# Kernel optimization log

Measured on AMD Instinct MI355X. Metric: run time of the kernel, lower is better.

Reference implementation:

```python
import jax, jax.numpy as jnp
import numpy as np

B, N, D, NH, MAXLEN = 2, 2048, 1024, 16, 2048
HD = D // NH

def srel_skew(x):
    # x: [B, H, n, n] -> music-transformer skew
    b, h, n, _ = x.shape
    v = jnp.pad(x, ((0, 0), (0, 0), (0, 0), (1, 0)))  # pad last dim left
    return v.reshape(b, h, n + 1, n)[:, :, :n, :]

def split_head(x):
    # [B, n, D] -> [B, H, n, HD]
    b, n, _ = x.shape
    return x.reshape(b, n, NH, HD).transpose(0, 2, 1, 3)

def setup_inputs() -> dict:
    key = jax.random.key(0)
    ks = jax.random.split(key, 7)
    scale = 0.02
    return {
        "x": jax.random.normal(ks[0], (B, N, D), dtype=jnp.float32),
        "Wq": jax.random.normal(ks[1], (D, D), dtype=jnp.float32) * scale,
        "Wk": jax.random.normal(ks[2], (D, D), dtype=jnp.float32) * scale,
        "Wv": jax.random.normal(ks[3], (D, D), dtype=jnp.float32) * scale,
        "Wp": jax.random.normal(ks[4], (D, D), dtype=jnp.float32) * scale,
        "bp": jnp.zeros((D,), dtype=jnp.float32),
        "rel_embed": jax.random.normal(ks[5], (MAXLEN, D), dtype=jnp.float32) * scale,
    }

def reference(x, Wq, Wk, Wv, Wp, bp, rel_embed):
    b, n, d = x.shape
    qx = split_head(x @ Wq.T)  # [B,H,n,HD]
    kx = split_head(x @ Wk.T)
    vx = split_head(x @ Wv.T)
    # relative distance embeddings for last n positions
    ns = jnp.arange(n) + (MAXLEN - n)
    ex = rel_embed[ns].reshape(n, NH, HD).transpose(1, 0, 2)  # [H,n,HD]
    srel = srel_skew(jnp.einsum('bhnd,hmd->bhnm', qx, ex))  # [B,H,n,n]
    inv_dim = 1.0 / np.sqrt(d / NH)
    qk = (jnp.einsum('bhnd,bhmd->bhnm', qx, kx) + srel) * inv_dim
    mask = 1e9 * jnp.triu(jnp.ones((n, n), dtype=x.dtype), 1)
    atten = jax.nn.softmax(qk - mask, axis=-1)
    out = jnp.einsum('bhnm,bhmd->bhnd', atten, vx).transpose(0, 2, 1, 3).reshape(b, n, d)
    return out @ Wp.T + bp
```

## Files before the change

kernel.cpp:

```cpp
#include <hip/hip_runtime.h>

typedef __attribute__((ext_vector_type(8))) short short8;
typedef __attribute__((ext_vector_type(4))) short s16x4;
typedef __attribute__((ext_vector_type(4))) float f32x4;
typedef unsigned short u16t;
typedef unsigned int u32t;

#define MFMA16(a,b,c) __builtin_amdgcn_mfma_f32_16x16x32_bf16((a),(b),(c),0,0,0)

__device__ __forceinline__ f32x4 mfma16x16(s16x4 a, s16x4 b, f32x4 c) {
#if __has_builtin(__builtin_amdgcn_mfma_f32_16x16x16bf16_1k)
  return __builtin_amdgcn_mfma_f32_16x16x16bf16_1k(a, b, c, 0, 0, 0);
#else
  __asm__("v_mfma_f32_16x16x16_bf16 %0, %1, %2, %0" : "+v"(c) : "v"(a), "v"(b));
  return c;
#endif
}

constexpr int Bc = 2, Nc = 2048, Dc = 1024, NHc = 16, HDc = 64;
constexpr int EStride = Nc + 80;

__device__ __forceinline__ u16t f2bf(float f) {
  union { float f; u32t u; } v; v.f = f;
  u32t r = v.u + 0x7FFFu + ((v.u >> 16) & 1u);
  return (u16t)(r >> 16);
}
#if __has_builtin(__builtin_amdgcn_cvt_pk_bf16_f32)
__device__ __forceinline__ u32t pk2(float a, float b) {
  auto r = __builtin_amdgcn_cvt_pk_bf16_f32(a, b);
  return __builtin_bit_cast(u32t, r);
}
#else
__device__ __forceinline__ u32t pk2(float a, float b) {
  u32t ua = __builtin_bit_cast(u32t, a);
  u32t ub = __builtin_bit_cast(u32t, b);
  return ((ua + 0x8000u) >> 16) | ((ub + 0x8000u) & 0xFFFF0000u);
}
#endif
__device__ __forceinline__ s16x4 pk4(float a, float b, float c, float d) {
  union { u32t u[2]; s16x4 s; } r;
  r.u[0] = pk2(a, b); r.u[1] = pk2(c, d);
  return r.s;
}

__device__ __forceinline__ s16x4 lo4(short8 v) {
  return __builtin_shufflevector(v, v, 0, 1, 2, 3);
}
__device__ __forceinline__ s16x4 hi4(short8 v) {
  return __builtin_shufflevector(v, v, 4, 5, 6, 7);
}

__device__ __forceinline__ void gld16(const u16t* g, u16t* l) {
  __builtin_amdgcn_global_load_lds(
      (const __attribute__((address_space(1))) unsigned int*)(g),
      (__attribute__((address_space(3))) unsigned int*)(l), 16, 0, 0);
}

__device__ __forceinline__ void cvt4(const float* s, u16t* d) {
  f32x4 v = *(const f32x4*)s;
  u32t* dp = (u32t*)d;
  dp[0] = pk2(v[0], v[1]); dp[1] = pk2(v[2], v[3]);
}

__global__ __launch_bounds__(256) void cvt_all(
    const float* __restrict__ x, const float* __restrict__ wq,
    const float* __restrict__ wk, const float* __restrict__ wv,
    const float* __restrict__ wp, const float* __restrict__ rel,
    u16t* __restrict__ xb, u16t* __restrict__ wqb, u16t* __restrict__ wkb,
    u16t* __restrict__ wvb, u16t* __restrict__ wpb, u16t* __restrict__ Eb) {
  int i = blockIdx.x * 256 + threadIdx.x;
  if (i < 1048576) {
    cvt4(x + (size_t)i * 4, xb + (size_t)i * 4);
  } else if (i < 2097152) {
    int r = i - 1048576;
    int w = r >> 18;
    int k = (r & 262143) * 4;
    const float* s = (w == 0) ? wq : (w == 1) ? wk : (w == 2) ? wv : wp;
    u16t* d = (w == 0) ? wqb : (w == 1) ? wkb : (w == 2) ? wvb : wpb;
    cvt4(s + k, d + k);
  } else if (i < 2621440) {
    int r = i - 2097152;
    int flat = r * 4;
    int h = flat >> 17;
    int rem = flat & 131071;
    int m = rem >> 6, d = rem & 63;
    cvt4(rel + (size_t)m * Dc + h * HDc + d,
         Eb + ((size_t)h * EStride + m) * HDc + d);
  } else {
    int r = i - 2621440;
    int flat = r * 4;
    int h = flat / 5120;
    int rem = flat - h * 5120;
    int pr = rem >> 6, d = rem & 63;
    u32t* dp = (u32t*)(Eb + ((size_t)h * EStride + Nc + pr) * HDc + d);
    dp[0] = 0; dp[1] = 0;
  }
}

__global__ __launch_bounds__(256, 3) void gemm_qkv(const u16t* __restrict__ A,
    const u16t* __restrict__ Wq, const u16t* __restrict__ Wk,
    const u16t* __restrict__ Wv, u16t* __restrict__ Qb,
    u16t* __restrict__ Kb, u16t* __restrict__ Vt) {
  __shared__ u16t lA[128 * 32];
  __shared__ u16t lB[128 * 32];
  const int y = blockIdx.y, which = y >> 3;
  const u16t* W = (which == 0) ? Wq : (which == 1) ? Wk : Wv;
  const float sc = 0.18033688011112042f;
  const int m0 = blockIdx.x * 128, n0 = (y & 7) * 128;
  const int t = threadIdx.x, wave = t >> 6, lane = t & 63;
  const int l15 = lane & 15, q4 = lane >> 4, wm = wave & 1, wn = wave >> 1;
  const int srow = wave * 16 + (lane >> 2);
  const int scol = (lane & 3) * 8;

  f32x4 acc[4][4];
  for (int i = 0; i < 4; i++)
    for (int j = 0; j < 4; j++)
      for (int r = 0; r < 4; r++) acc[i][j][r] = 0.f;

  for (int k0 = 0; k0 < Dc; k0 += 32) {
    __syncthreads();
    for (int r = 0; r < 2; r++) {
      int row = srow + r * 64;
      gld16(A + (size_t)(m0 + row) * Dc + k0 + scol, lA + wave * 512 + r * 2048);
      gld16(W + (size_t)(n0 + row) * Dc + k0 + scol, lB + wave * 512 + r * 2048);
    }
    __syncthreads();
    short8 af[4], bf[4];
    for (int i = 0; i < 4; i++) {
      af[i] = *(const short8*)(&lA[(wm * 64 + i * 16 + l15) * 32 + q4 * 8]);
      bf[i] = *(const short8*)(&lB[(wn * 64 + i * 16 + l15) * 32 + q4 * 8]);
    }
    for (int mi = 0; mi < 4; mi++)
      for (int ni = 0; ni < 4; ni++)
        acc[mi][ni] = MFMA16(af[mi], bf[ni], acc[mi][ni]);
  }

  if (which == 0) {
    for (int mi = 0; mi < 4; mi++)
      for (int ni = 0; ni < 4; ni++)
        for (int rg = 0; rg < 4; rg++) {
          int gm = m0 + wm * 64 + mi * 16 + q4 * 4 + rg;
          int gn = n0 + wn * 64 + ni * 16 + l15;
          int b = gm >> 11, n = gm & 2047, h = gn >> 6, hd = gn & 63;
          Qb[(((size_t)(b * NHc + h) * Nc + n) * HDc) + hd] =
              f2bf(acc[mi][ni][rg] * sc);
        }
  } else if (which == 1) {
    for (int mi = 0; mi < 4; mi++)
      for (int ni = 0; ni < 4; ni++)
        for (int rg = 0; rg < 4; rg++) {
          int gm = m0 + wm * 64 + mi * 16 + q4 * 4 + rg;
          int gn = n0 + wn * 64 + ni * 16 + l15;
          int b = gm >> 11, n = gm & 2047, h = gn >> 6, hd = gn & 63;
          size_t off = (size_t)(b * NHc + h) * Nc * HDc
                     + (size_t)(n >> 6) * 4096
                     + ((((n >> 4) & 3) * 2 + (hd >> 5)) * 512)
                     + (((hd >> 3) & 3) * 128) + ((n & 15) * 8) + (hd & 7);
          Kb[off] = f2bf(acc[mi][ni][rg]);
        }
  } else {
    for (int mi = 0; mi < 4; mi++)
      for (int ni = 0; ni < 4; ni++) {
        int gm = m0 + wm * 64 + mi * 16 + q4 * 4;
        int gn = n0 + wn * 64 + ni * 16 + l15;
        int b = gm >> 11, n = gm & 2047, h = gn >> 6, hd = gn & 63;
        s16x4 pkv = pk4(acc[mi][ni][0], acc[mi][ni][1],
                        acc[mi][ni][2], acc[mi][ni][3]);
        size_t off = (size_t)(b * NHc + h) * Nc * HDc
                   + (size_t)(n >> 6) * 4096
                   + (((hd >> 4) * 2 + ((n >> 5) & 1)) * 512)
                   + (((n >> 2) & 3) * 128) + ((hd & 15) * 8)
                   + (((n >> 4) & 1) * 4);
        *(s16x4*)(&Vt[off]) = pkv;
      }
  }
}

__global__ __launch_bounds__(256, 2) void gemm_proj(const u16t* __restrict__ A,
    const u16t* __restrict__ W, float* __restrict__ outf,
    const float* __restrict__ bias) {
  __shared__ u16t lA[64 * 32];
  __shared__ u16t lB[128 * 32];
  const int m0 = blockIdx.x * 64, n0 = blockIdx.y * 128;
  const int t = threadIdx.x, wave = t >> 6, lane = t & 63;
  const int l15 = lane & 15, q4 = lane >> 4, wm = wave & 1, wn = wave >> 1;
  const int srow = wave * 16 + (lane >> 2);
  const int scol = (lane & 3) * 8;

  f32x4 acc[2][4];
  for (int i = 0; i < 2; i++)
    for (int j = 0; j < 4; j++)
      for (int r = 0; r < 4; r++) acc[i][j][r] = 0.f;

  for (int k0 = 0; k0 < Dc; k0 += 32) {
    __syncthreads();
    gld16(A + (size_t)(m0 + srow) * Dc + k0 + scol, lA + wave * 512);
    for (int r = 0; r < 2; r++) {
      int row = srow + r * 64;
      gld16(W + (size_t)(n0 + row) * Dc + k0 + scol, lB + wave * 512 + r * 2048);
    }
    __syncthreads();
    short8 af[2], bf[4];
    for (int i = 0; i < 2; i++)
      af[i] = *(const short8*)(&lA[(wm * 32 + i * 16 + l15) * 32 + q4 * 8]);
    for (int i = 0; i < 4; i++)
      bf[i] = *(const short8*)(&lB[(wn * 64 + i * 16 + l15) * 32 + q4 * 8]);
    for (int mi = 0; mi < 2; mi++)
      for (int ni = 0; ni < 4; ni++)
        acc[mi][ni] = MFMA16(af[mi], bf[ni], acc[mi][ni]);
  }

  for (int mi = 0; mi < 2; mi++)
    for (int ni = 0; ni < 4; ni++)
      for (int rg = 0; rg < 4; rg++) {
        int gm = m0 + wm * 32 + mi * 16 + q4 * 4 + rg;
        int gn = n0 + wn * 64 + ni * 16 + l15;
        outf[(size_t)gm * Dc + gn] = acc[mi][ni][rg] + bias[gn];
      }
}

__global__ __launch_bounds__(256, 4) void attn(const u16t* __restrict__ Qb,
                                               const u16t* __restrict__ Kb,
                                               const u16t* __restrict__ Vt,
                                               const u16t* __restrict__ Eb,
                                               u16t* __restrict__ AO) {
  __shared__ u16t lE[128 * 72];
  __shared__ float Ps[4][16 * 84];

  const int bid = blockIdx.x;
  const int cu = bid & 255, k = bid >> 8;
  const int qi = cu >> 3;
  const int bh = ((cu & 7) << 2) | k;
  const int b = bh >> 4, h = bh & 15;

  const u16t* Qh = Qb + (size_t)(b * NHc + h) * Nc * HDc;
  const u16t* Kh = Kb + (size_t)(b * NHc + h) * Nc * HDc;
  const u16t* Vh = Vt + (size_t)(b * NHc + h) * Nc * HDc;
  const u16t* Eh = Eb + (size_t)h * EStride * HDc;

  const int t = threadIdx.x, wave = t >> 6, lane = t & 63, l15 = lane & 15, q4 = lane >> 4;
  const int tbase = (3 - wave) * 16;
  const int Tm = wave * 16 + l15;
  float* Pw = Ps[wave];

  const int sr = t >> 3, sc8 = (t & 7) * 8;
  const int sr2 = sr + 32;

  const int r0 = qi * 64;
  const int rw = r0 + wave * 16;

  short8 qf[2], qsf[2];
  {
    int r = rw + l15;
    int rs = r - 1; if (rs < 0) rs = 0;
    for (int kh = 0; kh < 2; kh++) {
      qf[kh]  = *(const short8*)(Qh + (size_t)r * HDc + kh * 32 + q4 * 8);
      qsf[kh] = *(const short8*)(Qh + (size_t)rs * HDc + kh * 32 + q4 * 8);
    }
  }

  f32x4 accO[4];
  f32x4 l4;
  for (int rg = 0; rg < 4; rg++) l4[rg] = 0.f;
  for (int dt = 0; dt < 4; dt++)
    for (int rg = 0; rg < 4; rg++) accO[dt][rg] = 0.f;

  auto body = [&](int j, bool last) {
    const u16t* Kt = Kh + (size_t)j * 4096;
    const u16t* Vj = Vh + (size_t)j * 4096;
    short8 kf[8], vf[8];
#pragma unroll
    for (int i = 0; i < 8; i++)
      kf[i] = *(const short8*)(Kt + i * 512 + lane * 8);
#pragma unroll
    for (int i = 0; i < 8; i++)
      vf[i] = *(const short8*)(Vj + i * 512 + lane * 8);

    const int rot = (j & 1) << 6;
    const int pbase = tbase + l15 + rot;
#pragma unroll
    for (int pt = 0; pt < 5; pt++) {
      f32x4 ap;
      ap[0] = 0.f; ap[1] = 0.f; ap[2] = 0.f; ap[3] = 0.f;
#pragma unroll
      for (int kh = 0; kh < 2; kh++) {
        int prow = (pbase + pt * 16) & 127;
        short8 efr = *(const short8*)(&lE[prow * 72 + kh * 32 + q4 * 8]);
        ap = MFMA16(efr, qsf[kh], ap);
      }
      *(f32x4*)(&Pw[l15 * 84 + pt * 16 + q4 * 4]) = ap;
    }
    f32x4 accS[4];
    for (int ct = 0; ct < 4; ct++)
      for (int rg = 0; rg < 4; rg++) accS[ct][rg] = 0.f;
#pragma unroll
    for (int kh = 0; kh < 2; kh++)
#pragma unroll
      for (int ct = 0; ct < 4; ct++)
        accS[ct] = MFMA16(kf[ct * 2 + kh], qf[kh], accS[ct]);

    __asm__ volatile("s_waitcnt lgkmcnt(0)" ::: "memory");
    const int rbase = l15 * 83 + q4 * 4 + 15;
    float pv[4][4];
    for (int ct = 0; ct < 4; ct++)
      for (int rg = 0; rg < 4; rg++) {
        float s = accS[ct][rg] + Pw[rbase + ct * 16 + rg];
        if (last && (ct * 16 + q4 * 4 + rg) > Tm) s = -1e30f;
        float p = exp2f(s);
        l4[rg] += p;
        pv[ct][rg] = p;
      }
    __asm__ volatile("" ::: "memory");
    s16x4 bq[4];
    for (int ks = 0; ks < 4; ks++)
      bq[ks] = pk4(pv[ks][0], pv[ks][1], pv[ks][2], pv[ks][3]);
#pragma unroll
    for (int dt = 0; dt < 4; dt++)
#pragma unroll
      for (int ks = 0; ks < 4; ks++) {
        s16x4 vfr = (ks & 1) ? hi4(vf[dt * 2 + (ks >> 1)])
                             : lo4(vf[dt * 2 + (ks >> 1)]);
        accO[dt] = mfma16x16(vfr, bq[ks], accO[dt]);
      }
  };

  {
    const int ebase0 = Nc - 63 - r0;
    for (int i = 0; i < 4; i++) {
      int cc = t + i * 256;
      int s = cc >> 3, c8 = (cc & 7) * 8;
      *(f32x4*)(&lE[s * 72 + c8]) =
          *(const f32x4*)(Eh + (size_t)(ebase0 + s) * HDc + c8);
    }
  }

  for (int j = 0; j < qi; j++) {
    __syncthreads();
    const int ebn = 64 * (j + 1) - r0 + (Nc - 63) + 64;
    f32x4 pE0 = *(const f32x4*)(Eh + (size_t)(ebn + sr) * HDc + sc8);
    f32x4 pE1 = *(const f32x4*)(Eh + (size_t)(ebn + sr2) * HDc + sc8);

    body(j, false);

    __syncthreads();
    int ph0 = (sr + 64 * j) & 127;
    int ph1 = (sr2 + 64 * j) & 127;
    *(f32x4*)(&lE[ph0 * 72 + sc8]) = pE0;
    *(f32x4*)(&lE[ph1 * 72 + sc8]) = pE1;
  }

  __syncthreads();
  body(qi, true);

  float l_p = (l4[0] + l4[1]) + (l4[2] + l4[3]);
  float l2 = l_p + __shfl_xor(l_p, 16);
  float lt = l2 + __shfl_xor(l2, 32);
  float inv = 1.f / lt;
  {
    int r = rw + l15;
    u16t* dst = AO + (size_t)(b * Nc + r) * Dc + h * HDc + q4 * 4;
    for (int dt = 0; dt < 4; dt++) {
      s16x4 o = pk4(accO[dt][0] * inv, accO[dt][1] * inv,
                    accO[dt][2] * inv, accO[dt][3] * inv);
      *(s16x4*)(dst + dt * 16) = o;
    }
  }
}

extern "C" void kernel_launch(void* const* d_in, const int* in_sizes, int n_in,
                              void* d_out, int out_size, void* d_ws, size_t ws_size,
                              hipStream_t stream) {
  (void)in_sizes; (void)n_in; (void)out_size; (void)ws_size;
  const float* x   = (const float*)d_in[0];
  const float* Wq  = (const float*)d_in[1];
  const float* Wk  = (const float*)d_in[2];
  const float* Wv  = (const float*)d_in[3];
  const float* Wp  = (const float*)d_in[4];
  const float* bp  = (const float*)d_in[5];
  const float* rel = (const float*)d_in[6];
  float* out = (float*)d_out;

  char* ws = (char*)d_ws;
  u16t* xb  = (u16t*)(ws);
  u16t* wqb = (u16t*)(ws + 8388608);
  u16t* wkb = (u16t*)(ws + 10485760);
  u16t* wvb = (u16t*)(ws + 12582912);
  u16t* wpb = (u16t*)(ws + 14680064);
  u16t* Eb  = (u16t*)(ws + 16777216);
  u16t* Qb  = (u16t*)(ws + 21233664);
  u16t* Kb  = (u16t*)(ws + 29622272);
  u16t* Vtb = (u16t*)(ws + 38010880);
  u16t* AOb = (u16t*)(ws + 46399488);

  cvt_all<<<10320, 256, 0, stream>>>(x, Wq, Wk, Wv, Wp, rel,
                                     xb, wqb, wkb, wvb, wpb, Eb);
  gemm_qkv<<<dim3(32, 24), 256, 0, stream>>>(xb, wqb, wkb, wvb, Qb, Kb, Vtb);
  attn<<<dim3(1024), 256, 0, stream>>>(Qb, Kb, Vtb, Eb, AOb);
  gemm_proj<<<dim3(64, 8), 256, 0, stream>>>(AOb, wpb, out, bp);
}
```

Measured before the change: 232.8 us.

## Drop shared-memory E staging, read E fragments from global and prefetch K

Removes the shared-memory ring buffer for the relative-position embedding and its two block-wide barriers per iteration. Each wave now loads its E fragments straight from global or L2. K fragments for the next tile are prefetched into registers while the current scores are computed. The block order is remapped so the longest causal rows (largest qi) launch first, and the occupancy hint drops from 4 to 3 blocks per SIMD to make room for the extra registers. The trade is redundant global E traffic across waves and lower occupancy in exchange for no syncs and better latency hiding.

```diff
diff --git a/kernel.cpp b/kernel.cpp
--- a/kernel.cpp
+++ b/kernel.cpp
@@ -219,18 +219,16 @@
       }
 }
 
-__global__ __launch_bounds__(256, 4) void attn(const u16t* __restrict__ Qb,
+__global__ __launch_bounds__(256, 3) void attn(const u16t* __restrict__ Qb,
                                                const u16t* __restrict__ Kb,
                                                const u16t* __restrict__ Vt,
                                                const u16t* __restrict__ Eb,
                                                u16t* __restrict__ AO) {
-  __shared__ u16t lE[128 * 72];
   __shared__ float Ps[4][16 * 84];
 
   const int bid = blockIdx.x;
-  const int cu = bid & 255, k = bid >> 8;
-  const int qi = cu >> 3;
-  const int bh = ((cu & 7) << 2) | k;
+  const int qi = 31 - (bid >> 5);
+  const int bh = bid & 31;
   const int b = bh >> 4, h = bh & 15;
 
   const u16t* Qh = Qb + (size_t)(b * NHc + h) * Nc * HDc;
@@ -243,11 +241,9 @@
   const int Tm = wave * 16 + l15;
   float* Pw = Ps[wave];
 
-  const int sr = t >> 3, sc8 = (t & 7) * 8;
-  const int sr2 = sr + 32;
-
   const int r0 = qi * 64;
   const int rw = r0 + wave * 16;
+  const int eb0 = (Nc - 63 - r0) + tbase + l15;
 
   short8 qf[2], qsf[2];
   {
@@ -265,55 +261,66 @@
   for (int dt = 0; dt < 4; dt++)
     for (int rg = 0; rg < 4; rg++) accO[dt][rg] = 0.f;
 
-  auto body = [&](int j, bool last) {
-    const u16t* Kt = Kh + (size_t)j * 4096;
+  short8 kf[8];
+#pragma unroll
+  for (int i = 0; i < 8; i++)
+    kf[i] = *(const short8*)(Kh + i * 512 + lane * 8);
+
+  auto body = [&](int j, bool last, bool pf) {
     const u16t* Vj = Vh + (size_t)j * 4096;
-    short8 kf[8], vf[8];
-#pragma unroll
-    for (int i = 0; i < 8; i++)
-      kf[i] = *(const short8*)(Kt + i * 512 + lane * 8);
+    short8 vf[8];
 #pragma unroll
     for (int i = 0; i < 8; i++)
       vf[i] = *(const short8*)(Vj + i * 512 + lane * 8);
 
-    const int rot = (j & 1) << 6;
-    const int pbase = tbase + l15 + rot;
+    f32x4 accS[4];
+    for (int ct = 0; ct < 4; ct++)
+      for (int rg = 0; rg < 4; rg++) accS[ct][rg] = 0.f;
+#pragma unroll
+    for (int kh = 0; kh < 2; kh++)
+#pragma unroll
+      for (int ct = 0; ct < 4; ct++)
+        accS[ct] = MFMA16(kf[ct * 2 + kh], qf[kh], accS[ct]);
+
+    if (pf) {
+      const u16t* Kn = Kh + (size_t)(j + 1) * 4096;
+#pragma unroll
+      for (int i = 0; i < 8; i++)
+        kf[i] = *(const short8*)(Kn + i * 512 + lane * 8);
+    }
+
+    const int erb = eb0 + 64 * j;
 #pragma unroll
     for (int pt = 0; pt < 5; pt++) {
       f32x4 ap;
       ap[0] = 0.f; ap[1] = 0.f; ap[2] = 0.f; ap[3] = 0.f;
 #pragma unroll
       for (int kh = 0; kh < 2; kh++) {
-        int prow = (pbase + pt * 16) & 127;
-        short8 efr = *(const short8*)(&lE[prow * 72 + kh * 32 + q4 * 8]);
+        short8 efr = *(const short8*)(Eh + (size_t)(erb + pt * 16) * HDc +
+                                      kh * 32 + q4 * 8);
         ap = MFMA16(efr, qsf[kh], ap);
       }
       *(f32x4*)(&Pw[l15 * 84 + pt * 16 + q4 * 4]) = ap;
     }
-    f32x4 accS[4];
-    for (int ct = 0; ct < 4; ct++)
-      for (int rg = 0; rg < 4; rg++) accS[ct][rg] = 0.f;
-#pragma unroll
-    for (int kh = 0; kh < 2; kh++)
-#pragma unroll
-      for (int ct = 0; ct < 4; ct++)
-        accS[ct] = MFMA16(kf[ct * 2 + kh], qf[kh], accS[ct]);
 
     __asm__ volatile("s_waitcnt lgkmcnt(0)" ::: "memory");
+    __builtin_amdgcn_sched_barrier(0);
     const int rbase = l15 * 83 + q4 * 4 + 15;
-    float pv[4][4];
-    for (int ct = 0; ct < 4; ct++)
+    s16x4 bq[4];
+#pragma unroll
+    for (int ct = 0; ct < 4; ct++) {
+      float pv[4];
+#pragma unroll
       for (int rg = 0; rg < 4; rg++) {
         float s = accS[ct][rg] + Pw[rbase + ct * 16 + rg];
         if (last && (ct * 16 + q4 * 4 + rg) > Tm) s = -1e30f;
         float p = exp2f(s);
         l4[rg] += p;
-        pv[ct][rg] = p;
-      }
+        pv[rg] = p;
+      }
+      bq[ct] = pk4(pv[0], pv[1], pv[2], pv[3]);
+    }
     __asm__ volatile("" ::: "memory");
-    s16x4 bq[4];
-    for (int ks = 0; ks < 4; ks++)
-      bq[ks] = pk4(pv[ks][0], pv[ks][1], pv[ks][2], pv[ks][3]);
 #pragma unroll
     for (int dt = 0; dt < 4; dt++)
 #pragma unroll
@@ -324,33 +331,8 @@
       }
   };
 
-  {
-    const int ebase0 = Nc - 63 - r0;
-    for (int i = 0; i < 4; i++) {
-      int cc = t + i * 256;
-      int s = cc >> 3, c8 = (cc & 7) * 8;
-      *(f32x4*)(&lE[s * 72 + c8]) =
-          *(const f32x4*)(Eh + (size_t)(ebase0 + s) * HDc + c8);
-    }
-  }
-
-  for (int j = 0; j < qi; j++) {
-    __syncthreads();
-    const int ebn = 64 * (j + 1) - r0 + (Nc - 63) + 64;
-    f32x4 pE0 = *(const f32x4*)(Eh + (size_t)(ebn + sr) * HDc + sc8);
-    f32x4 pE1 = *(const f32x4*)(Eh + (size_t)(ebn + sr2) * HDc + sc8);
-
-    body(j, false);
-
-    __syncthreads();
-    int ph0 = (sr + 64 * j) & 127;
-    int ph1 = (sr2 + 64 * j) & 127;
-    *(f32x4*)(&lE[ph0 * 72 + sc8]) = pE0;
-    *(f32x4*)(&lE[ph1 * 72 + sc8]) = pE1;
-  }
-
-  __syncthreads();
-  body(qi, true);
+  for (int j = 0; j < qi; j++) body(j, false, true);
+  body(qi, true, false);
 
   float l_p = (l4[0] + l4[1]) + (l4[2] + l4[3]);
   float l2 = l_p + __shfl_xor(l_p, 16);
```

Measured after the change: 259.7 us. +11.5%, slower.
